# Performance work log

Measured on AMD Instinct MI355X. Metric: run time of the kernel, lower is better.

Reference implementation:

```python
import jax, jax.numpy as jnp
import numpy as np

NUM_HEADS = 8
NUM_GROUPS = 32  # min(C//4, 32) for C=512
EPS = 1e-6       # flax GroupNorm default


def setup_inputs() -> dict:
    key = jax.random.key(0)
    ks = jax.random.split(key, 3)
    B, H, W, D, C = 2, 16, 16, 16, 512
    x = jax.random.normal(ks[0], (B, H, W, D, C), dtype=jnp.float32)
    w_qkv = jax.random.normal(ks[1], (C, 3 * C), dtype=jnp.float32) / np.sqrt(C)
    w_proj = jax.random.normal(ks[2], (C, C), dtype=jnp.float32) / np.sqrt(C)
    return {
        "x": x,
        "gn_scale": jnp.ones((C,), jnp.float32),
        "gn_bias": jnp.zeros((C,), jnp.float32),
        "w_qkv": w_qkv,
        "b_qkv": jnp.zeros((3 * C,), jnp.float32),
        "w_proj": w_proj,
        "b_proj": jnp.zeros((C,), jnp.float32),
    }


def group_norm(x, scale, bias):
    # x: [B, S, C]; normalize within each of NUM_GROUPS channel groups over (S, group-channels)
    B, S, C = x.shape
    xg = x.reshape(B, S, NUM_GROUPS, C // NUM_GROUPS)
    mean = jnp.mean(xg, axis=(1, 3), keepdims=True)
    var = jnp.var(xg, axis=(1, 3), keepdims=True)
    xn = (xg - mean) * jax.lax.rsqrt(var + EPS)
    return xn.reshape(B, S, C) * scale + bias


def reference(x, gn_scale, gn_bias, w_qkv, b_qkv, w_proj, b_proj):
    B, H, W, D, C = x.shape
    S = H * W * D
    hd = C // NUM_HEADS
    xf = x.reshape(B, S, C)
    q_in = group_norm(xf, gn_scale, gn_bias)
    # 1x1x1 conv == per-position dense
    qkv = q_in @ w_qkv + b_qkv                      # [B, S, 3C]
    qkv = qkv.reshape(B, S, NUM_HEADS, 3 * hd)
    q, k, v = jnp.split(qkv, 3, axis=-1)            # each [B, S, nh, hd]
    scale = 1.0 / jnp.sqrt(jnp.asarray(hd, x.dtype))
    logits = jnp.einsum('btnh,bfnh->bnft', k, q * scale)  # [B, nh, S, S]
    weights = jax.nn.softmax(logits, axis=-1)
    h = jnp.einsum('bnft,btnh->bfnh', weights, v)   # [B, S, nh, hd]
    h = h.reshape(B, S, C) @ w_proj + b_proj
    return h.reshape(x.shape) + x
```

## Files before the change

kernel.cpp:

```cpp
#include <hip/hip_runtime.h>

typedef __attribute__((ext_vector_type(8))) short short8;
typedef __attribute__((ext_vector_type(4))) float f32x4;
typedef __attribute__((ext_vector_type(16))) float f32x16;

#define S_LEN 4096
#define C_DIM 512
#define NH 8
#define HD 64
#define NG 32
#define GS 16
#define LOG2E 1.44269504088896340736f

__device__ __forceinline__ unsigned short f2bf(float f) {
  union { float f; unsigned int u; } v; v.f = f;
  unsigned int r = v.u + 0x7fffu + ((v.u >> 16) & 1u);
  return (unsigned short)(r >> 16);
}

__device__ __forceinline__ float bf2f(unsigned short s) {
  union { unsigned u; float f; } v; v.u = (unsigned)s << 16;
  return v.f;
}

__device__ __forceinline__ float fexp2(float x) {
  float r;
  asm("v_exp_f32 %0, %1" : "=v"(r) : "v"(x));
  return r;
}

__device__ __forceinline__ unsigned pk_bf16(float a, float b) {
  unsigned r;
  asm("v_cvt_pk_bf16_f32 %0, %1, %2" : "=v"(r) : "v"(a), "v"(b));
  return r;
}

__device__ __forceinline__ void pl_swap(unsigned& a, unsigned& b) {
  asm("v_permlane32_swap_b32 %0, %1" : "+v"(a), "+v"(b));
}

__device__ __forceinline__ void gload_lds16(const void* g, void* l) {
  __builtin_amdgcn_global_load_lds((const __attribute__((address_space(1))) void*)g,
                                   (__attribute__((address_space(3))) void*)l, 16, 0, 0);
}

__global__ __launch_bounds__(256) void prep_kernel(const float* __restrict__ x,
                                                   float* __restrict__ partials,
                                                   const float* __restrict__ w_qkv,
                                                   unsigned short* __restrict__ wqkvT,
                                                   const float* __restrict__ w_proj,
                                                   unsigned short* __restrict__ wprojT) {
  __shared__ float tile[32][33];
  __shared__ float r1[4], r2[4];
  int bid = blockIdx.x;
  if (bid < 256) {
    int bg = bid >> 2, chunk = bid & 3;
    int b = bg >> 5, g = bg & 31;
    const float* xp = x + (size_t)b * S_LEN * C_DIM + g * GS;
    float s1 = 0.f, s2 = 0.f;
    for (int i = threadIdx.x; i < 1024 * 4; i += 256) {
      int s = chunk * 1024 + (i >> 2), c4 = i & 3;
      float4 v = *(const float4*)&xp[(size_t)s * C_DIM + c4 * 4];
      s1 += v.x + v.y + v.z + v.w;
      s2 += v.x * v.x + v.y * v.y + v.z * v.z + v.w * v.w;
    }
    for (int off = 1; off < 64; off <<= 1) {
      s1 += __shfl_xor(s1, off);
      s2 += __shfl_xor(s2, off);
    }
    int w = threadIdx.x >> 6;
    if ((threadIdx.x & 63) == 0) { r1[w] = s1; r2[w] = s2; }
    __syncthreads();
    if (threadIdx.x == 0) {
      partials[bg * 8 + chunk * 2]     = r1[0] + r1[1] + r1[2] + r1[3];
      partials[bg * 8 + chunk * 2 + 1] = r2[0] + r2[1] + r2[2] + r2[3];
    }
    return;
  }
  const float* src; unsigned short* dst; int K, N, n0, k0;
  if (bid < 1024) {
    int t = bid - 256;  src = w_qkv;  dst = wqkvT;  K = 512; N = 1536;
    n0 = (t % 48) * 32; k0 = (t / 48) * 32;
  } else {
    int t = bid - 1024; src = w_proj; dst = wprojT; K = 512; N = 512;
    n0 = (t % 16) * 32; k0 = (t / 16) * 32;
  }
  int c = threadIdx.x & 31, r0 = threadIdx.x >> 5;
  for (int i = 0; i < 4; ++i) {
    int r = r0 + i * 8;
    tile[r][c] = src[(size_t)(k0 + r) * N + n0 + c];
  }
  __syncthreads();
  for (int i = 0; i < 4; ++i) {
    int r = r0 + i * 8;
    dst[(size_t)(n0 + r) * K + k0 + c] = f2bf(tile[c][r]);
  }
}

__global__ __launch_bounds__(256) void gn_apply_kernel(const float* __restrict__ x,
                                                       const float* __restrict__ partials,
                                                       const float* __restrict__ scale,
                                                       const float* __restrict__ bias,
                                                       unsigned short* __restrict__ out) {
  int idx = blockIdx.x * 256 + threadIdx.x;
  int e = idx * 4;
  int c = e & (C_DIM - 1);
  int bs = e >> 9;
  int b = bs >> 12;
  int grp = b * NG + (c >> 4);
  float s1 = partials[grp * 8] + partials[grp * 8 + 2] + partials[grp * 8 + 4] + partials[grp * 8 + 6];
  float s2 = partials[grp * 8 + 1] + partials[grp * 8 + 3] + partials[grp * 8 + 5] + partials[grp * 8 + 7];
  const float invN = 1.0f / (float)(S_LEN * GS);
  float mean = s1 * invN;
  float var = s2 * invN - mean * mean;
  float rstd = rsqrtf(var + 1e-6f);
  float4 v = *(const float4*)&x[e];
  ushort4 o;
  o.x = f2bf((v.x - mean) * rstd * scale[c]     + bias[c]);
  o.y = f2bf((v.y - mean) * rstd * scale[c + 1] + bias[c + 1]);
  o.z = f2bf((v.z - mean) * rstd * scale[c + 2] + bias[c + 2]);
  o.w = f2bf((v.w - mean) * rstd * scale[c + 3] + bias[c + 3]);
  *(ushort4*)&out[e] = o;
}

template <int MODE>
__global__ __launch_bounds__(256) void gemm_kernel(const unsigned short* __restrict__ A,
                                                   const unsigned short* __restrict__ Bt,
                                                   const float* __restrict__ bias,
                                                   unsigned short* __restrict__ qh,
                                                   unsigned short* __restrict__ kh,
                                                   unsigned short* __restrict__ vh,
                                                   const float* __restrict__ resid,
                                                   float* __restrict__ outf) {
  __shared__ unsigned char Alds[16384];
  __shared__ unsigned char Blds[16384];
  int tid = threadIdx.x, lane = tid & 63, w = tid >> 6;
  int li = lane & 15, g = lane >> 4;
  int wr = (w >> 1) * 64, wc = (w & 1) * 64;
  int m0 = blockIdx.y * 128, n0 = blockIdx.x * 128;

  int srow = tid >> 3;
  int colS = (tid & 7) * 16;
  int sc   = colS ^ ((srow & 7) << 4);
  const char* aSrc = (const char*)A + (size_t)(m0 + srow) * 1024 + sc;
  const char* bSrc = (const char*)Bt + (size_t)(n0 + srow) * 1024 + sc;

  f32x4 acc[4][4];
  for (int i = 0; i < 4; ++i)
    for (int j = 0; j < 4; ++j) acc[i][j] = (f32x4){0.f, 0.f, 0.f, 0.f};

  for (int k0 = 0; k0 < 512; k0 += 64) {
#pragma unroll
    for (int r = 0; r < 4; ++r) {
      gload_lds16(aSrc + (size_t)r * 32 * 1024 + k0 * 2, &Alds[r * 4096 + tid * 16]);
      gload_lds16(bSrc + (size_t)r * 32 * 1024 + k0 * 2, &Blds[r * 4096 + tid * 16]);
    }
    asm volatile("s_waitcnt vmcnt(0)" ::: "memory");
    __builtin_amdgcn_s_barrier();

#pragma unroll
    for (int ks = 0; ks < 2; ++ks) {
      short8 af[4], bfm[4];
#pragma unroll
      for (int mi = 0; mi < 4; ++mi) {
        int row = wr + mi * 16 + li;
        af[mi] = *(const short8*)&Alds[row * 128 + ((ks * 64 + g * 16) ^ ((row & 7) << 4))];
      }
#pragma unroll
      for (int ni = 0; ni < 4; ++ni) {
        int row = wc + ni * 16 + li;
        bfm[ni] = *(const short8*)&Blds[row * 128 + ((ks * 64 + g * 16) ^ ((row & 7) << 4))];
      }
#pragma unroll
      for (int mi = 0; mi < 4; ++mi)
#pragma unroll
        for (int ni = 0; ni < 4; ++ni)
          acc[mi][ni] = __builtin_amdgcn_mfma_f32_16x16x32_bf16(af[mi], bfm[ni], acc[mi][ni], 0, 0, 0);
    }
    __syncthreads();
  }

  if (MODE == 0) {
    for (int ni = 0; ni < 4; ++ni) {
      int n = n0 + wc + ni * 16 + li;
      float bn = bias[n];
      int head = n / 192;
      int rem = n - head * 192;
      int part = rem >> 6;
      int h = rem & 63;
      if (part == 2) {
        for (int mi = 0; mi < 4; ++mi) {
          int m = m0 + wr + mi * 16 + g * 4;
          int b = m >> 12, s = m & 4095;
          size_t idx = ((size_t)(b * NH + head) * HD + h) * S_LEN + s;
          ushort4 val;
          val.x = f2bf(acc[mi][ni][0] + bn);
          val.y = f2bf(acc[mi][ni][1] + bn);
          val.z = f2bf(acc[mi][ni][2] + bn);
          val.w = f2bf(acc[mi][ni][3] + bn);
          *(ushort4*)&vh[idx] = val;
        }
      } else {
        unsigned short* dst = part == 0 ? qh : kh;
        float mul = part == 0 ? 0.125f * LOG2E : 1.0f;
        for (int mi = 0; mi < 4; ++mi)
          for (int j = 0; j < 4; ++j) {
            int m = m0 + wr + mi * 16 + g * 4 + j;
            int b = m >> 12, s = m & 4095;
            dst[((size_t)(b * NH + head) * S_LEN + s) * HD + h] = f2bf((acc[mi][ni][j] + bn) * mul);
          }
      }
    }
  } else {
    for (int ni = 0; ni < 4; ++ni) {
      int n = n0 + wc + ni * 16 + li;
      float bn = bias[n];
      for (int mi = 0; mi < 4; ++mi)
        for (int j = 0; j < 4; ++j) {
          int m = m0 + wr + mi * 16 + g * 4 + j;
          size_t off = (size_t)m * C_DIM + n;
          outf[off] = acc[mi][ni][j] + bn + resid[off];
        }
    }
  }
}

__global__ __launch_bounds__(256) void gemm_proj_kernel(const unsigned short* __restrict__ opart,
                                                        const float* __restrict__ lpart,
                                                        const unsigned short* __restrict__ Bt,
                                                        const float* __restrict__ bias,
                                                        const float* __restrict__ resid,
                                                        float* __restrict__ outf) {
  __shared__ unsigned char Alds[16384];
  __shared__ unsigned char Blds[16384];
  __shared__ float linv[8][128];
  int tid = threadIdx.x, lane = tid & 63, w = tid >> 6;
  int li = lane & 15, g = lane >> 4;
  int wr = (w >> 1) * 64, wc = (w & 1) * 64;
  int m0 = blockIdx.y * 128, n0 = blockIdx.x * 128;
  int b_ = m0 >> 12;
  int s0 = m0 & 4095;

  int srow = tid >> 3;
  int colS = (tid & 7) * 16;
  int sc   = colS ^ ((srow & 7) << 4);
  const char* bSrc = (const char*)Bt + (size_t)(n0 + srow) * 1024 + sc;

#pragma unroll
  for (int i = 0; i < 4; ++i) {
    int e = tid + i * 256;
    int hd_ = e >> 7, r = e & 127;
    size_t rowA = (size_t)((b_ * NH + hd_) * 2) * S_LEN + s0 + r;
    linv[hd_][r] = 1.0f / (lpart[rowA] + lpart[rowA + S_LEN]);
  }
  __syncthreads();

  int tr = tid >> 1, hf2 = tid & 1;
  size_t rowBase = ((size_t)(b_ * NH) * 2) * S_LEN + s0 + tr;

  f32x4 acc[4][4];
  for (int i = 0; i < 4; ++i)
    for (int j = 0; j < 4; ++j) acc[i][j] = (f32x4){0.f, 0.f, 0.f, 0.f};

  for (int k0 = 0; k0 < 512; k0 += 64) {
    int head = k0 >> 6;
#pragma unroll
    for (int r = 0; r < 4; ++r)
      gload_lds16(bSrc + (size_t)r * 32 * 1024 + k0 * 2, &Blds[r * 4096 + tid * 16]);

    size_t rowA = rowBase + (size_t)head * 2 * S_LEN;
    const unsigned short* pA0 = opart + rowA * 64 + hf2 * 32;
    const unsigned short* pA1 = opart + (rowA + S_LEN) * 64 + hf2 * 32;
    float inv = linv[head][tr];
#pragma unroll
    for (int q = 0; q < 4; ++q) {
      short8 x = *(const short8*)&pA0[q * 8];
      short8 y = *(const short8*)&pA1[q * 8];
      union { unsigned u[4]; short8 v; } d;
#pragma unroll
      for (int p = 0; p < 4; ++p) {
        float f0 = (bf2f((unsigned short)x[2 * p])     + bf2f((unsigned short)y[2 * p]))     * inv;
        float f1 = (bf2f((unsigned short)x[2 * p + 1]) + bf2f((unsigned short)y[2 * p + 1])) * inv;
        d.u[p] = pk_bf16(f0, f1);
      }
      int cc = hf2 * 64 + q * 16;
      *(short8*)&Alds[tr * 128 + (cc ^ ((tr & 7) << 4))] = d.v;
    }
    __syncthreads();

#pragma unroll
    for (int ks = 0; ks < 2; ++ks) {
      short8 af[4], bfm[4];
#pragma unroll
      for (int mi = 0; mi < 4; ++mi) {
        int row = wr + mi * 16 + li;
        af[mi] = *(const short8*)&Alds[row * 128 + ((ks * 64 + g * 16) ^ ((row & 7) << 4))];
      }
#pragma unroll
      for (int ni = 0; ni < 4; ++ni) {
        int row = wc + ni * 16 + li;
        bfm[ni] = *(const short8*)&Blds[row * 128 + ((ks * 64 + g * 16) ^ ((row & 7) << 4))];
      }
#pragma unroll
      for (int mi = 0; mi < 4; ++mi)
#pragma unroll
        for (int ni = 0; ni < 4; ++ni)
          acc[mi][ni] = __builtin_amdgcn_mfma_f32_16x16x32_bf16(af[mi], bfm[ni], acc[mi][ni], 0, 0, 0);
    }
    __syncthreads();
  }

  for (int ni = 0; ni < 4; ++ni) {
    int n = n0 + wc + ni * 16 + li;
    float bn = bias[n];
    for (int mi = 0; mi < 4; ++mi)
      for (int j = 0; j < 4; ++j) {
        int m = m0 + wr + mi * 16 + g * 4 + j;
        size_t off = (size_t)m * C_DIM + n;
        outf[off] = acc[mi][ni][j] + bn + resid[off];
      }
  }
}

template <int SPLIT>
__global__ __launch_bounds__(256, 4) void attn_kernel(const unsigned short* __restrict__ qh,
                                                      const unsigned short* __restrict__ kh,
                                                      const unsigned short* __restrict__ vt,
                                                      unsigned short* __restrict__ ob,
                                                      unsigned short* __restrict__ opart,
                                                      float* __restrict__ lpart) {
  __shared__ unsigned char Kt[3 * 4096];
  __shared__ unsigned char Vt[3 * 4096];
  int bn = blockIdx.y;
  int half = SPLIT > 1 ? blockIdx.z : 0;
  int tid = threadIdx.x, lane = tid & 63, wv = tid >> 6;
  int r32 = lane & 31, hi_ = lane >> 5;
  int q0 = blockIdx.x * 128 + wv * 32;
  const int NT = S_LEN / 32 / SPLIT;
  const unsigned short* qp = qh + (size_t)bn * S_LEN * HD;
  const char* kp = (const char*)(kh + (size_t)bn * S_LEN * HD);
  const char* vp = (const char*)(vt + (size_t)bn * HD * S_LEN);

  int srow  = wv * 8 + (lane >> 3);
  int scolS = (lane & 7) * 16;
  int sc    = scolS ^ ((srow & 7) << 4);
  const char* kSrc = kp + (size_t)srow * 128 + sc + (size_t)half * (S_LEN / SPLIT) * 128;
  int vh_ = srow + ((sc >> 6) << 5);
  const char* vSrc = vp + (size_t)vh_ * (S_LEN * 2) + (sc & 63) + (size_t)half * (S_LEN / SPLIT) * 2;

  short8 qf[4];
#pragma unroll
  for (int ks = 0; ks < 4; ++ks)
    qf[ks] = *(const short8*)&qp[(size_t)(q0 + r32) * HD + ks * 16 + hi_ * 8];

  union { unsigned u[4]; short8 v; } ones;
#pragma unroll
  for (int i = 0; i < 4; ++i) ones.u[i] = 0x3F803F80u;

  f32x16 o0, o1, lacc, z16;
#pragma unroll
  for (int i = 0; i < 16; ++i) { o0[i] = 0.f; o1[i] = 0.f; lacc[i] = 0.f; z16[i] = 0.f; }

  int swzr = (r32 & 7) << 4;
  int sBase = wv * 1024;

  gload_lds16(kSrc, &Kt[sBase]);
  gload_lds16(vSrc, &Vt[sBase]);
  gload_lds16(kSrc + 32 * 128, &Kt[4096 + sBase]);
  gload_lds16(vSrc + 32 * 2,   &Vt[4096 + sBase]);
  asm volatile("s_waitcnt vmcnt(2)" ::: "memory");
  __builtin_amdgcn_s_barrier();

  int curO = 0, nxtO = 4096, nnO = 8192;
  for (int it = 0; it < NT; ++it) {
    bool more = (it + 2 < NT);
    if (more) {
      size_t t0n = (size_t)(it + 2) * 32;
      gload_lds16(kSrc + t0n * 128, &Kt[nnO + sBase]);
      gload_lds16(vSrc + t0n * 2,   &Vt[nnO + sBase]);
    }

    const unsigned char* Kr = &Kt[curO + r32 * 128];
    const unsigned char* Vr = &Vt[curO + r32 * 128];
    short8 kf[4], vf[4];
#pragma unroll
    for (int ks = 0; ks < 4; ++ks)
      kf[ks] = *(const short8*)&Kr[(ks * 32 + hi_ * 16) ^ swzr];
#pragma unroll
    for (int kk = 0; kk < 2; ++kk)
#pragma unroll
      for (int hf = 0; hf < 2; ++hf)
        vf[kk * 2 + hf] = *(const short8*)&Vr[(hf * 64 + kk * 32 + hi_ * 16) ^ swzr];

    f32x16 s = __builtin_amdgcn_mfma_f32_32x32x16_bf16(kf[0], qf[0], z16, 0, 0, 0);
#pragma unroll
    for (int ks = 1; ks < 4; ++ks)
      s = __builtin_amdgcn_mfma_f32_32x32x16_bf16(kf[ks], qf[ks], s, 0, 0, 0);

#pragma unroll
    for (int i = 0; i < 16; ++i) s[i] = fexp2(s[i]);

    unsigned pkv[8];
#pragma unroll
    for (int g2 = 0; g2 < 8; ++g2) pkv[g2] = pk_bf16(s[2 * g2], s[2 * g2 + 1]);
    pl_swap(pkv[0], pkv[2]); pl_swap(pkv[1], pkv[3]);
    pl_swap(pkv[4], pkv[6]); pl_swap(pkv[5], pkv[7]);
    union { unsigned u[4]; short8 v; } F0, F1;
    F0.u[0] = pkv[0]; F0.u[1] = pkv[1]; F0.u[2] = pkv[2]; F0.u[3] = pkv[3];
    F1.u[0] = pkv[4]; F1.u[1] = pkv[5]; F1.u[2] = pkv[6]; F1.u[3] = pkv[7];

    o0 = __builtin_amdgcn_mfma_f32_32x32x16_bf16(vf[0], F0.v, o0, 0, 0, 0);
    o1 = __builtin_amdgcn_mfma_f32_32x32x16_bf16(vf[1], F0.v, o1, 0, 0, 0);
    lacc = __builtin_amdgcn_mfma_f32_32x32x16_bf16(ones.v, F0.v, lacc, 0, 0, 0);
    o0 = __builtin_amdgcn_mfma_f32_32x32x16_bf16(vf[2], F1.v, o0, 0, 0, 0);
    o1 = __builtin_amdgcn_mfma_f32_32x32x16_bf16(vf[3], F1.v, o1, 0, 0, 0);
    lacc = __builtin_amdgcn_mfma_f32_32x32x16_bf16(ones.v, F1.v, lacc, 0, 0, 0);

    if (more) asm volatile("s_waitcnt vmcnt(2)" ::: "memory");
    else      asm volatile("s_waitcnt vmcnt(0)" ::: "memory");
    __builtin_amdgcn_s_barrier();
    int t = curO; curO = nxtO; nxtO = nnO; nnO = t;
  }

  if (SPLIT == 1) {
    float inv = 1.0f / lacc[0];
    int b = bn >> 3, n = bn & 7;
    size_t base = ((size_t)(b * S_LEN + q0 + r32)) * C_DIM + n * HD;
#pragma unroll
    for (int r = 0; r < 16; ++r) {
      int hrow = (r & 3) + 8 * (r >> 2) + 4 * hi_;
      ob[base + hrow]      = f2bf(o0[r] * inv);
      ob[base + 32 + hrow] = f2bf(o1[r] * inv);
    }
  } else {
    size_t row = (size_t)(bn * SPLIT + half) * S_LEN + q0 + r32;
    unsigned short* pp = opart + row * 64;
#pragma unroll
    for (int i = 0; i < 8; ++i) {
      int r = 2 * i;
      int hrow = (r & 3) + 8 * (r >> 2) + 4 * hi_;
      *(unsigned*)&pp[hrow]      = pk_bf16(o0[r], o0[r + 1]);
      *(unsigned*)&pp[32 + hrow] = pk_bf16(o1[r], o1[r + 1]);
    }
    if (!hi_) lpart[row] = lacc[0];
  }
}

extern "C" void kernel_launch(void* const* d_in, const int* in_sizes, int n_in,
                              void* d_out, int out_size, void* d_ws, size_t ws_size,
                              hipStream_t stream) {
  const float* x        = (const float*)d_in[0];
  const float* gn_scale = (const float*)d_in[1];
  const float* gn_bias  = (const float*)d_in[2];
  const float* w_qkv    = (const float*)d_in[3];
  const float* b_qkv    = (const float*)d_in[4];
  const float* w_proj   = (const float*)d_in[5];
  const float* b_proj   = (const float*)d_in[6];
  float* out = (float*)d_out;

  char* ws = (char*)d_ws;
  unsigned short* q_in   = (unsigned short*)(ws);
  unsigned short* wqkvT  = (unsigned short*)(ws + 8388608);
  unsigned short* wprojT = (unsigned short*)(ws + 9961472);
  unsigned short* qhb    = (unsigned short*)(ws + 10485760);
  unsigned short* khb    = (unsigned short*)(ws + 18874368);
  unsigned short* vtb    = (unsigned short*)(ws + 27262976);
  unsigned short* ahb    = (unsigned short*)(ws + 35651584);
  float* partials        = (float*)(ws + 44040192);
  float* lpart           = (float*)(ws + 44042240);
  unsigned short* opart  = (unsigned short*)(ws + 45090816);
  const size_t NEED2 = 45090816ull + (size_t)16 * 2 * S_LEN * 64 * 2;

  prep_kernel<<<1280, 256, 0, stream>>>(x, partials, w_qkv, wqkvT, w_proj, wprojT);
  gn_apply_kernel<<<4096, 256, 0, stream>>>(x, partials, gn_scale, gn_bias, q_in);
  gemm_kernel<0><<<dim3(12, 64), 256, 0, stream>>>(q_in, wqkvT, b_qkv, qhb, khb, vtb, nullptr, nullptr);
  if (ws_size >= NEED2) {
    attn_kernel<2><<<dim3(32, 16, 2), 256, 0, stream>>>(qhb, khb, vtb, nullptr, opart, lpart);
    gemm_proj_kernel<<<dim3(4, 64), 256, 0, stream>>>(opart, lpart, wprojT, b_proj, x, out);
  } else {
    attn_kernel<1><<<dim3(32, 16, 1), 256, 0, stream>>>(qhb, khb, vtb, ahb, nullptr, nullptr);
    gemm_kernel<1><<<dim3(4, 64), 256, 0, stream>>>(ahb, wprojT, b_proj, nullptr, nullptr, nullptr, x, out);
  }
}
```

Baseline: 151.5 us.

## Fuse GroupNorm apply into QKV GEMM and compute softmax row sums on VALU

Removes the separate GroupNorm-apply kernel and its bf16 intermediate buffer. The QKV GEMM now loads fp32 x directly, applies per-channel scale and shift precomputed into LDS, and writes bf16 into the swizzled A tile. Separately, the attention kernel drops the extra ones-matrix MFMAs used for the softmax denominator and instead sums the exponentials in registers, combining the two lane halves with a permlane swap. The tradeoffs are that x is re-read as fp32 by all 12 column blocks, which is twice the A-operand bytes of bf16, and the A loads no longer go asynchronously to LDS.

```diff
diff --git a/kernel.cpp b/kernel.cpp
--- a/kernel.cpp
+++ b/kernel.cpp
@@ -36,6 +36,9 @@
 }
 
 __device__ __forceinline__ void pl_swap(unsigned& a, unsigned& b) {
+  asm("v_permlane32_swap_b32 %0, %1" : "+v"(a), "+v"(b));
+}
+__device__ __forceinline__ void pl_swapf(float& a, float& b) {
   asm("v_permlane32_swap_b32 %0, %1" : "+v"(a), "+v"(b));
 }
 
@@ -97,41 +100,137 @@
   }
 }
 
-__global__ __launch_bounds__(256) void gn_apply_kernel(const float* __restrict__ x,
+__global__ __launch_bounds__(256) void gemm_qkv_kernel(const float* __restrict__ x,
                                                        const float* __restrict__ partials,
-                                                       const float* __restrict__ scale,
-                                                       const float* __restrict__ bias,
-                                                       unsigned short* __restrict__ out) {
-  int idx = blockIdx.x * 256 + threadIdx.x;
-  int e = idx * 4;
-  int c = e & (C_DIM - 1);
-  int bs = e >> 9;
-  int b = bs >> 12;
-  int grp = b * NG + (c >> 4);
-  float s1 = partials[grp * 8] + partials[grp * 8 + 2] + partials[grp * 8 + 4] + partials[grp * 8 + 6];
-  float s2 = partials[grp * 8 + 1] + partials[grp * 8 + 3] + partials[grp * 8 + 5] + partials[grp * 8 + 7];
+                                                       const float* __restrict__ gscale,
+                                                       const float* __restrict__ gbias,
+                                                       const unsigned short* __restrict__ Bt,
+                                                       const float* __restrict__ qbias,
+                                                       unsigned short* __restrict__ qh,
+                                                       unsigned short* __restrict__ kh,
+                                                       unsigned short* __restrict__ vh) {
+  __shared__ unsigned char Alds[16384];
+  __shared__ unsigned char Blds[16384];
+  __shared__ float AsL[512], CsL[512];
+  int tid = threadIdx.x, lane = tid & 63, w = tid >> 6;
+  int li = lane & 15, g = lane >> 4;
+  int wr = (w >> 1) * 64, wc = (w & 1) * 64;
+  int m0 = blockIdx.y * 128, n0 = blockIdx.x * 128;
+  int b_ = m0 >> 12;
+
+  int srow = tid >> 3;
+  int colS = (tid & 7) * 16;
+  int sc   = colS ^ ((srow & 7) << 4);
+  const char* bSrc = (const char*)Bt + (size_t)(n0 + srow) * 1024 + sc;
+
   const float invN = 1.0f / (float)(S_LEN * GS);
-  float mean = s1 * invN;
-  float var = s2 * invN - mean * mean;
-  float rstd = rsqrtf(var + 1e-6f);
-  float4 v = *(const float4*)&x[e];
-  ushort4 o;
-  o.x = f2bf((v.x - mean) * rstd * scale[c]     + bias[c]);
-  o.y = f2bf((v.y - mean) * rstd * scale[c + 1] + bias[c + 1]);
-  o.z = f2bf((v.z - mean) * rstd * scale[c + 2] + bias[c + 2]);
-  o.w = f2bf((v.w - mean) * rstd * scale[c + 3] + bias[c + 3]);
-  *(ushort4*)&out[e] = o;
-}
-
-template <int MODE>
-__global__ __launch_bounds__(256) void gemm_kernel(const unsigned short* __restrict__ A,
-                                                   const unsigned short* __restrict__ Bt,
-                                                   const float* __restrict__ bias,
-                                                   unsigned short* __restrict__ qh,
-                                                   unsigned short* __restrict__ kh,
-                                                   unsigned short* __restrict__ vh,
-                                                   const float* __restrict__ resid,
-                                                   float* __restrict__ outf) {
+#pragma unroll
+  for (int i = 0; i < 2; ++i) {
+    int c = tid + i * 256;
+    int bg = b_ * NG + (c >> 4);
+    float s1 = partials[bg * 8] + partials[bg * 8 + 2] + partials[bg * 8 + 4] + partials[bg * 8 + 6];
+    float s2 = partials[bg * 8 + 1] + partials[bg * 8 + 3] + partials[bg * 8 + 5] + partials[bg * 8 + 7];
+    float mean = s1 * invN;
+    float var = s2 * invN - mean * mean;
+    float rstd = rsqrtf(var + 1e-6f);
+    float A_ = rstd * gscale[c];
+    AsL[c] = A_;
+    CsL[c] = gbias[c] - mean * A_;
+  }
+  __syncthreads();
+
+  int tr = tid >> 1, hf2 = tid & 1;
+  const float* xRow = x + (size_t)(m0 + tr) * C_DIM + hf2 * 32;
+
+  f32x4 acc[4][4];
+  for (int i = 0; i < 4; ++i)
+    for (int j = 0; j < 4; ++j) acc[i][j] = (f32x4){0.f, 0.f, 0.f, 0.f};
+
+  for (int k0 = 0; k0 < 512; k0 += 64) {
+    float4 xv[8];
+#pragma unroll
+    for (int q = 0; q < 8; ++q) xv[q] = *(const float4*)&xRow[k0 + q * 4];
+#pragma unroll
+    for (int r = 0; r < 4; ++r)
+      gload_lds16(bSrc + (size_t)r * 32 * 1024 + k0 * 2, &Blds[r * 4096 + tid * 16]);
+
+    int cbase = k0 + hf2 * 32;
+#pragma unroll
+    for (int q = 0; q < 4; ++q) {
+      union { unsigned u[4]; short8 v; } d;
+#pragma unroll
+      for (int p = 0; p < 2; ++p) {
+        int c = cbase + q * 8 + p * 4;
+        float4 A4 = *(const float4*)&AsL[c];
+        float4 C4 = *(const float4*)&CsL[c];
+        float4 vv = xv[2 * q + p];
+        d.u[p * 2]     = pk_bf16(vv.x * A4.x + C4.x, vv.y * A4.y + C4.y);
+        d.u[p * 2 + 1] = pk_bf16(vv.z * A4.z + C4.z, vv.w * A4.w + C4.w);
+      }
+      int cc = hf2 * 64 + q * 16;
+      *(short8*)&Alds[tr * 128 + (cc ^ ((tr & 7) << 4))] = d.v;
+    }
+    __syncthreads();
+
+#pragma unroll
+    for (int ks = 0; ks < 2; ++ks) {
+      short8 af[4], bfm[4];
+#pragma unroll
+      for (int mi = 0; mi < 4; ++mi) {
+        int row = wr + mi * 16 + li;
+        af[mi] = *(const short8*)&Alds[row * 128 + ((ks * 64 + g * 16) ^ ((row & 7) << 4))];
+      }
+#pragma unroll
+      for (int ni = 0; ni < 4; ++ni) {
+        int row = wc + ni * 16 + li;
+        bfm[ni] = *(const short8*)&Blds[row * 128 + ((ks * 64 + g * 16) ^ ((row & 7) << 4))];
+      }
+#pragma unroll
+      for (int mi = 0; mi < 4; ++mi)
+#pragma unroll
+        for (int ni = 0; ni < 4; ++ni)
+          acc[mi][ni] = __builtin_amdgcn_mfma_f32_16x16x32_bf16(af[mi], bfm[ni], acc[mi][ni], 0, 0, 0);
+    }
+    __syncthreads();
+  }
+
+  for (int ni = 0; ni < 4; ++ni) {
+    int n = n0 + wc + ni * 16 + li;
+    float bn = qbias[n];
+    int head = n / 192;
+    int rem = n - head * 192;
+    int part = rem >> 6;
+    int h = rem & 63;
+    if (part == 2) {
+      for (int mi = 0; mi < 4; ++mi) {
+        int m = m0 + wr + mi * 16 + g * 4;
+        int b = m >> 12, s = m & 4095;
+        size_t idx = ((size_t)(b * NH + head) * HD + h) * S_LEN + s;
+        ushort4 val;
+        val.x = f2bf(acc[mi][ni][0] + bn);
+        val.y = f2bf(acc[mi][ni][1] + bn);
+        val.z = f2bf(acc[mi][ni][2] + bn);
+        val.w = f2bf(acc[mi][ni][3] + bn);
+        *(ushort4*)&vh[idx] = val;
+      }
+    } else {
+      unsigned short* dst = part == 0 ? qh : kh;
+      float mul = part == 0 ? 0.125f * LOG2E : 1.0f;
+      for (int mi = 0; mi < 4; ++mi)
+        for (int j = 0; j < 4; ++j) {
+          int m = m0 + wr + mi * 16 + g * 4 + j;
+          int b = m >> 12, s = m & 4095;
+          dst[((size_t)(b * NH + head) * S_LEN + s) * HD + h] = f2bf((acc[mi][ni][j] + bn) * mul);
+        }
+    }
+  }
+}
+
+__global__ __launch_bounds__(256) void gemm_plain_kernel(const unsigned short* __restrict__ A,
+                                                         const unsigned short* __restrict__ Bt,
+                                                         const float* __restrict__ bias,
+                                                         const float* __restrict__ resid,
+                                                         float* __restrict__ outf) {
   __shared__ unsigned char Alds[16384];
   __shared__ unsigned char Blds[16384];
   int tid = threadIdx.x, lane = tid & 63, w = tid >> 6;
@@ -157,7 +256,6 @@
     }
     asm volatile("s_waitcnt vmcnt(0)" ::: "memory");
     __builtin_amdgcn_s_barrier();
-
 #pragma unroll
     for (int ks = 0; ks < 2; ++ks) {
       short8 af[4], bfm[4];
@@ -180,48 +278,15 @@
     __syncthreads();
   }
 
-  if (MODE == 0) {
-    for (int ni = 0; ni < 4; ++ni) {
-      int n = n0 + wc + ni * 16 + li;
-      float bn = bias[n];
-      int head = n / 192;
-      int rem = n - head * 192;
-      int part = rem >> 6;
-      int h = rem & 63;
-      if (part == 2) {
-        for (int mi = 0; mi < 4; ++mi) {
-          int m = m0 + wr + mi * 16 + g * 4;
-          int b = m >> 12, s = m & 4095;
-          size_t idx = ((size_t)(b * NH + head) * HD + h) * S_LEN + s;
-          ushort4 val;
-          val.x = f2bf(acc[mi][ni][0] + bn);
-          val.y = f2bf(acc[mi][ni][1] + bn);
-          val.z = f2bf(acc[mi][ni][2] + bn);
-          val.w = f2bf(acc[mi][ni][3] + bn);
-          *(ushort4*)&vh[idx] = val;
-        }
-      } else {
-        unsigned short* dst = part == 0 ? qh : kh;
-        float mul = part == 0 ? 0.125f * LOG2E : 1.0f;
-        for (int mi = 0; mi < 4; ++mi)
-          for (int j = 0; j < 4; ++j) {
-            int m = m0 + wr + mi * 16 + g * 4 + j;
-            int b = m >> 12, s = m & 4095;
-            dst[((size_t)(b * NH + head) * S_LEN + s) * HD + h] = f2bf((acc[mi][ni][j] + bn) * mul);
-          }
-      }
-    }
-  } else {
-    for (int ni = 0; ni < 4; ++ni) {
-      int n = n0 + wc + ni * 16 + li;
-      float bn = bias[n];
-      for (int mi = 0; mi < 4; ++mi)
-        for (int j = 0; j < 4; ++j) {
-          int m = m0 + wr + mi * 16 + g * 4 + j;
-          size_t off = (size_t)m * C_DIM + n;
-          outf[off] = acc[mi][ni][j] + bn + resid[off];
-        }
-    }
+  for (int ni = 0; ni < 4; ++ni) {
+    int n = n0 + wc + ni * 16 + li;
+    float bn = bias[n];
+    for (int mi = 0; mi < 4; ++mi)
+      for (int j = 0; j < 4; ++j) {
+        int m = m0 + wr + mi * 16 + g * 4 + j;
+        size_t off = (size_t)m * C_DIM + n;
+        outf[off] = acc[mi][ni][j] + bn + resid[off];
+      }
   }
 }
 
@@ -274,13 +339,13 @@
     float inv = linv[head][tr];
 #pragma unroll
     for (int q = 0; q < 4; ++q) {
-      short8 x = *(const short8*)&pA0[q * 8];
-      short8 y = *(const short8*)&pA1[q * 8];
+      short8 xx = *(const short8*)&pA0[q * 8];
+      short8 yy = *(const short8*)&pA1[q * 8];
       union { unsigned u[4]; short8 v; } d;
 #pragma unroll
       for (int p = 0; p < 4; ++p) {
-        float f0 = (bf2f((unsigned short)x[2 * p])     + bf2f((unsigned short)y[2 * p]))     * inv;
-        float f1 = (bf2f((unsigned short)x[2 * p + 1]) + bf2f((unsigned short)y[2 * p + 1])) * inv;
+        float f0 = (bf2f((unsigned short)xx[2 * p])     + bf2f((unsigned short)yy[2 * p]))     * inv;
+        float f1 = (bf2f((unsigned short)xx[2 * p + 1]) + bf2f((unsigned short)yy[2 * p + 1])) * inv;
         d.u[p] = pk_bf16(f0, f1);
       }
       int cc = hf2 * 64 + q * 16;
@@ -353,13 +418,10 @@
   for (int ks = 0; ks < 4; ++ks)
     qf[ks] = *(const short8*)&qp[(size_t)(q0 + r32) * HD + ks * 16 + hi_ * 8];
 
-  union { unsigned u[4]; short8 v; } ones;
-#pragma unroll
-  for (int i = 0; i < 4; ++i) ones.u[i] = 0x3F803F80u;
-
-  f32x16 o0, o1, lacc, z16;
-#pragma unroll
-  for (int i = 0; i < 16; ++i) { o0[i] = 0.f; o1[i] = 0.f; lacc[i] = 0.f; z16[i] = 0.f; }
+  f32x16 o0, o1, z16;
+#pragma unroll
+  for (int i = 0; i < 16; ++i) { o0[i] = 0.f; o1[i] = 0.f; z16[i] = 0.f; }
+  float lsum = 0.f;
 
   int swzr = (r32 & 7) << 4;
   int sBase = wv * 1024;
@@ -400,6 +462,12 @@
 #pragma unroll
     for (int i = 0; i < 16; ++i) s[i] = fexp2(s[i]);
 
+    float t0 = (s[0] + s[1]) + (s[2] + s[3]);
+    float t1 = (s[4] + s[5]) + (s[6] + s[7]);
+    float t2 = (s[8] + s[9]) + (s[10] + s[11]);
+    float t3 = (s[12] + s[13]) + (s[14] + s[15]);
+    lsum += (t0 + t1) + (t2 + t3);
+
     unsigned pkv[8];
 #pragma unroll
     for (int g2 = 0; g2 < 8; ++g2) pkv[g2] = pk_bf16(s[2 * g2], s[2 * g2 + 1]);
@@ -411,10 +479,8 @@
 
     o0 = __builtin_amdgcn_mfma_f32_32x32x16_bf16(vf[0], F0.v, o0, 0, 0, 0);
     o1 = __builtin_amdgcn_mfma_f32_32x32x16_bf16(vf[1], F0.v, o1, 0, 0, 0);
-    lacc = __builtin_amdgcn_mfma_f32_32x32x16_bf16(ones.v, F0.v, lacc, 0, 0, 0);
     o0 = __builtin_amdgcn_mfma_f32_32x32x16_bf16(vf[2], F1.v, o0, 0, 0, 0);
     o1 = __builtin_amdgcn_mfma_f32_32x32x16_bf16(vf[3], F1.v, o1, 0, 0, 0);
-    lacc = __builtin_amdgcn_mfma_f32_32x32x16_bf16(ones.v, F1.v, lacc, 0, 0, 0);
 
     if (more) asm volatile("s_waitcnt vmcnt(2)" ::: "memory");
     else      asm volatile("s_waitcnt vmcnt(0)" ::: "memory");
@@ -422,8 +488,10 @@
     int t = curO; curO = nxtO; nxtO = nnO; nnO = t;
   }
 
+  { float c2 = lsum; pl_swapf(lsum, c2); lsum += c2; }
+
   if (SPLIT == 1) {
-    float inv = 1.0f / lacc[0];
+    float inv = 1.0f / lsum;
     int b = bn >> 3, n = bn & 7;
     size_t base = ((size_t)(b * S_LEN + q0 + r32)) * C_DIM + n * HD;
 #pragma unroll
@@ -442,7 +510,7 @@
       *(unsigned*)&pp[hrow]      = pk_bf16(o0[r], o0[r + 1]);
       *(unsigned*)&pp[32 + hrow] = pk_bf16(o1[r], o1[r + 1]);
     }
-    if (!hi_) lpart[row] = lacc[0];
+    if (!hi_) lpart[row] = lsum;
   }
 }
 
@@ -459,7 +527,6 @@
   float* out = (float*)d_out;
 
   char* ws = (char*)d_ws;
-  unsigned short* q_in   = (unsigned short*)(ws);
   unsigned short* wqkvT  = (unsigned short*)(ws + 8388608);
   unsigned short* wprojT = (unsigned short*)(ws + 9961472);
   unsigned short* qhb    = (unsigned short*)(ws + 10485760);
@@ -472,13 +539,13 @@
   const size_t NEED2 = 45090816ull + (size_t)16 * 2 * S_LEN * 64 * 2;
 
   prep_kernel<<<1280, 256, 0, stream>>>(x, partials, w_qkv, wqkvT, w_proj, wprojT);
-  gn_apply_kernel<<<4096, 256, 0, stream>>>(x, partials, gn_scale, gn_bias, q_in);
-  gemm_kernel<0><<<dim3(12, 64), 256, 0, stream>>>(q_in, wqkvT, b_qkv, qhb, khb, vtb, nullptr, nullptr);
+  gemm_qkv_kernel<<<dim3(12, 64), 256, 0, stream>>>(x, partials, gn_scale, gn_bias, wqkvT, b_qkv,
+                                                    qhb, khb, vtb);
   if (ws_size >= NEED2) {
     attn_kernel<2><<<dim3(32, 16, 2), 256, 0, stream>>>(qhb, khb, vtb, nullptr, opart, lpart);
     gemm_proj_kernel<<<dim3(4, 64), 256, 0, stream>>>(opart, lpart, wprojT, b_proj, x, out);
   } else {
     attn_kernel<1><<<dim3(32, 16, 1), 256, 0, stream>>>(qhb, khb, vtb, ahb, nullptr, nullptr);
-    gemm_kernel<1><<<dim3(4, 64), 256, 0, stream>>>(ahb, wprojT, b_proj, nullptr, nullptr, nullptr, x, out);
-  }
-}
+    gemm_plain_kernel<<<dim3(4, 64), 256, 0, stream>>>(ahb, wprojT, b_proj, x, out);
+  }
+}
```

After: 164.5 us. 8.6% more time.
